# Kernel optimization log

Hardware: AMD Instinct MI355X
Metric: run time of the kernel (lower is better)

The kernel has to match this reference:

```python
import jax, jax.numpy as jnp
import numpy as np

NU, NM, E, H = 200000, 40000, 2000000, 64


def setup_inputs() -> dict:
    key = jax.random.key(0)
    ks = jax.random.split(key, 16)
    inp = {}
    inp["x_user"] = jnp.arange(NU, dtype=jnp.int32)
    inp["x_movie"] = jnp.arange(NM, dtype=jnp.int32)
    # user->movie ratings and the reverse edge type (same edges, flipped)
    src_u = jax.random.randint(ks[0], (E,), 0, NU, dtype=jnp.int32)
    dst_m = jax.random.randint(ks[1], (E,), 0, NM, dtype=jnp.int32)
    inp["edge_src_um"], inp["edge_dst_um"] = src_u, dst_m
    inp["edge_src_mu"], inp["edge_dst_mu"] = dst_m, src_u
    inp["user_table"] = jax.random.normal(ks[2], (NU, H), dtype=jnp.float32)
    inp["movie_table"] = jax.random.normal(ks[3], (NM, H), dtype=jnp.float32)
    s = 1.0 / np.sqrt(H)
    wnames = ["Wl1_um", "Wr1_um", "Wl1_mu", "Wr1_mu", "Wl2_um", "Wr2_um", "Wl2_mu", "Wr2_mu"]
    for i, n in enumerate(wnames):
        inp[n] = jax.random.uniform(ks[4 + i], (H, H), minval=-s, maxval=s, dtype=jnp.float32)
    for i, n in enumerate(["b1_um", "b1_mu", "b2_um", "b2_mu"]):
        inp[n] = jax.random.uniform(ks[12 + i], (H,), minval=-s, maxval=s, dtype=jnp.float32)
    return inp


def sage_conv(x_src, x_dst, src, dst, Wl, Wr, b, n_dst):
    """PyG SAGEConv (bipartite, aggr='mean'): lin_l(mean_j x_j) + lin_r(x_i) + b."""
    msg = x_src[src]                                            # [E, H] gather
    agg = jax.ops.segment_sum(msg, dst, num_segments=n_dst)     # [n_dst, H]
    cnt = jax.ops.segment_sum(jnp.ones((src.shape[0], 1), x_src.dtype), dst,
                              num_segments=n_dst)
    agg = agg / jnp.maximum(cnt, 1.0)                           # mean, 0 for isolated nodes
    return agg @ Wl + x_dst @ Wr + b


def reference(x_user, x_movie, edge_src_um, edge_dst_um, edge_src_mu, edge_dst_mu,
              user_table, movie_table,
              Wl1_um, Wr1_um, Wl1_mu, Wr1_mu, Wl2_um, Wr2_um, Wl2_mu, Wr2_mu,
              b1_um, b1_mu, b2_um, b2_mu):
    u0 = user_table[x_user]    # [NU, H]
    m0 = movie_table[x_movie]  # [NM, H]
    # layer 1 (per edge type; each node type has one incoming edge type, aggr='sum' trivial)
    m1 = jax.nn.relu(sage_conv(u0, m0, edge_src_um, edge_dst_um, Wl1_um, Wr1_um, b1_um, NM))
    u1 = jax.nn.relu(sage_conv(m0, u0, edge_src_mu, edge_dst_mu, Wl1_mu, Wr1_mu, b1_mu, NU))
    # layer 2
    m2 = sage_conv(u1, m1, edge_src_um, edge_dst_um, Wl2_um, Wr2_um, b2_um, NM)
    u2 = sage_conv(m1, u1, edge_src_mu, edge_dst_mu, Wl2_mu, Wr2_mu, b2_mu, NU)
    return (u2, m2)
```

## Files before the change

kernel.cpp:

```cpp
#include <hip/hip_runtime.h>

#define HDIM 64
#define CAP_M 96
#define CAP_U 32
#define OVF_MAX 65536
#define NBIN 512
#define NBLK 2048

typedef __attribute__((ext_vector_type(8))) short bf16x8;
typedef __attribute__((ext_vector_type(4))) float f32x4;

__device__ __forceinline__ float bf2f(unsigned short u) {
  unsigned int x = ((unsigned int)u) << 16;
  return __uint_as_float(x);
}
__device__ __forceinline__ unsigned short f2bf(float f) {
  unsigned int x = __float_as_uint(f);
  unsigned int r = (x + 0x7FFFu + ((x >> 16) & 1u)) >> 16;
  return (unsigned short)r;
}

__device__ __forceinline__ int bin_lo(int b, int Nd) {
  return (int)(((long long)b * Nd + NBIN - 1) >> 9);
}

__global__ __launch_bounds__(256) void k_init(int* __restrict__ meta, int nmeta,
                                              const float* __restrict__ ut,
                                              unsigned short* __restrict__ ub, int n8u,
                                              const float* __restrict__ mt,
                                              unsigned short* __restrict__ mb, int n8m) {
  int bid = blockIdx.x;
  if (bid < 512) {
    int i = bid * 256 + threadIdx.x;
    for (int j = i; j < nmeta; j += 512 * 256) meta[j] = 0;
  } else if (bid < 512 + 2048) {
    int i = (bid - 512) * 256 + threadIdx.x;
    for (int j = i; j < n8u; j += 2048 * 256) {
      const float4* p = (const float4*)(ut + (size_t)j * 8);
      float4 a = p[0], b = p[1];
      uint4 o;
      o.x = (unsigned int)f2bf(a.x) | ((unsigned int)f2bf(a.y) << 16);
      o.y = (unsigned int)f2bf(a.z) | ((unsigned int)f2bf(a.w) << 16);
      o.z = (unsigned int)f2bf(b.x) | ((unsigned int)f2bf(b.y) << 16);
      o.w = (unsigned int)f2bf(b.z) | ((unsigned int)f2bf(b.w) << 16);
      *(uint4*)(ub + (size_t)j * 8) = o;
    }
  } else {
    int i = (bid - 512 - 2048) * 256 + threadIdx.x;
    for (int j = i; j < n8m; j += 512 * 256) {
      const float4* p = (const float4*)(mt + (size_t)j * 8);
      float4 a = p[0], b = p[1];
      uint4 o;
      o.x = (unsigned int)f2bf(a.x) | ((unsigned int)f2bf(a.y) << 16);
      o.y = (unsigned int)f2bf(a.z) | ((unsigned int)f2bf(a.w) << 16);
      o.z = (unsigned int)f2bf(b.x) | ((unsigned int)f2bf(b.y) << 16);
      o.w = (unsigned int)f2bf(b.z) | ((unsigned int)f2bf(b.w) << 16);
      *(uint4*)(mb + (size_t)j * 8) = o;
    }
  }
}

__global__ __launch_bounds__(256) void k_hist2(const int* __restrict__ srcU,
                                               const int* __restrict__ dstM,
                                               int E, int NMd, int NUd,
                                               int* __restrict__ ghM,
                                               int* __restrict__ ghU) {
  __shared__ int hM[NBIN];
  __shared__ int hU[NBIN];
  int t = threadIdx.x;
  hM[t] = 0; hM[t + 256] = 0;
  hU[t] = 0; hU[t + 256] = 0;
  __syncthreads();
  int e4 = (E + 3) >> 2;
  int c4 = (e4 + NBLK - 1) / NBLK;
  int clen = c4 << 2;
  int s = blockIdx.x * clen;
  int epos = s + clen; if (epos > E) epos = E;
  for (int i = s + 4 * t; i < epos; i += 1024) {
    int n = epos - i; if (n > 4) n = 4;
    if (n == 4) {
      int4 d4 = *(const int4*)&dstM[i];
      int4 s4 = *(const int4*)&srcU[i];
      atomicAdd(&hM[(int)((long long)d4.x * NBIN / NMd)], 1);
      atomicAdd(&hM[(int)((long long)d4.y * NBIN / NMd)], 1);
      atomicAdd(&hM[(int)((long long)d4.z * NBIN / NMd)], 1);
      atomicAdd(&hM[(int)((long long)d4.w * NBIN / NMd)], 1);
      atomicAdd(&hU[(int)((long long)s4.x * NBIN / NUd)], 1);
      atomicAdd(&hU[(int)((long long)s4.y * NBIN / NUd)], 1);
      atomicAdd(&hU[(int)((long long)s4.z * NBIN / NUd)], 1);
      atomicAdd(&hU[(int)((long long)s4.w * NBIN / NUd)], 1);
    } else {
      for (int j = 0; j < n; ++j) {
        atomicAdd(&hM[(int)((long long)dstM[i + j] * NBIN / NMd)], 1);
        atomicAdd(&hU[(int)((long long)srcU[i + j] * NBIN / NUd)], 1);
      }
    }
  }
  __syncthreads();
  ghM[(size_t)t * NBLK + blockIdx.x] = hM[t];
  ghM[(size_t)(t + 256) * NBLK + blockIdx.x] = hM[t + 256];
  ghU[(size_t)t * NBLK + blockIdx.x] = hU[t];
  ghU[(size_t)(t + 256) * NBLK + blockIdx.x] = hU[t + 256];
}

__global__ void k_block_sum(const int* __restrict__ in, int* __restrict__ part, int n) {
  __shared__ int s[256];
  int b = blockIdx.x, t = threadIdx.x;
  int base = b * 1024;
  int v = 0;
  for (int i = t; i < 1024; i += 256) {
    int idx = base + i;
    if (idx < n) v += in[idx];
  }
  s[t] = v;
  __syncthreads();
  for (int o = 128; o > 0; o >>= 1) {
    if (t < o) s[t] += s[t + o];
    __syncthreads();
  }
  if (t == 0) part[b] = s[0];
}

__global__ void k_scan_part4(int* __restrict__ part, int nb) {
  __shared__ int s[256];
  int t = threadIdx.x;
  int v[4];
  int sum = 0;
#pragma unroll
  for (int i = 0; i < 4; ++i) {
    int idx = t * 4 + i;
    v[i] = (idx < nb) ? part[idx] : 0;
    sum += v[i];
  }
  s[t] = sum;
  __syncthreads();
  for (int o = 1; o < 256; o <<= 1) {
    int u = (t >= o) ? s[t - o] : 0;
    __syncthreads();
    s[t] += u;
    __syncthreads();
  }
  int excl = s[t] - sum;
#pragma unroll
  for (int i = 0; i < 4; ++i) {
    int idx = t * 4 + i;
    if (idx < nb) { int tmp = v[i]; part[idx] = excl; excl += tmp; }
  }
}

__global__ void k_scan_final(const int* __restrict__ in, const int* __restrict__ part,
                             int* __restrict__ out, int n) {
  __shared__ int s[256];
  int b = blockIdx.x, t = threadIdx.x;
  int base = b * 1024 + t * 4;
  int a[4];
#pragma unroll
  for (int i = 0; i < 4; i++) a[i] = (base + i < n) ? in[base + i] : 0;
  int tsum = a[0] + a[1] + a[2] + a[3];
  s[t] = tsum;
  __syncthreads();
  for (int o = 1; o < 256; o <<= 1) {
    int u = (t >= o) ? s[t - o] : 0;
    __syncthreads();
    s[t] += u;
    __syncthreads();
  }
  int excl = s[t] - tsum + part[b];
#pragma unroll
  for (int i = 0; i < 4; i++) {
    if (base + i < n) out[base + i] = excl;
    excl += a[i];
  }
}

__global__ __launch_bounds__(256) void k_scatter2(const int* __restrict__ srcU,
                                                  const int* __restrict__ dstM,
                                                  int E, int NMd, int NUd,
                                                  const int* __restrict__ offsM,
                                                  const int* __restrict__ offsU,
                                                  unsigned int* __restrict__ binnedM,
                                                  unsigned int* __restrict__ binnedU) {
  __shared__ int lcM[NBIN];
  __shared__ int lcU[NBIN];
  int t = threadIdx.x;
  lcM[t] = offsM[(size_t)t * NBLK + blockIdx.x];
  lcM[t + 256] = offsM[(size_t)(t + 256) * NBLK + blockIdx.x];
  lcU[t] = offsU[(size_t)t * NBLK + blockIdx.x];
  lcU[t + 256] = offsU[(size_t)(t + 256) * NBLK + blockIdx.x];
  __syncthreads();
  int e4 = (E + 3) >> 2;
  int c4 = (e4 + NBLK - 1) / NBLK;
  int clen = c4 << 2;
  int s = blockIdx.x * clen;
  int epos = s + clen; if (epos > E) epos = E;
  for (int i = s + 4 * t; i < epos; i += 1024) {
    int n = epos - i; if (n > 4) n = 4;
    if (n == 4) {
      int4 d4 = *(const int4*)&dstM[i];
      int4 s4 = *(const int4*)&srcU[i];
#pragma unroll
      for (int k = 0; k < 4; ++k) {
        int dd = (k == 0) ? d4.x : (k == 1) ? d4.y : (k == 2) ? d4.z : d4.w;
        int ss = (k == 0) ? s4.x : (k == 1) ? s4.y : (k == 2) ? s4.z : s4.w;
        int bm = (int)((long long)dd * NBIN / NMd);
        int pm = atomicAdd(&lcM[bm], 1);
        binnedM[pm] = ((unsigned int)(dd - bin_lo(bm, NMd)) << 18) | (unsigned int)ss;
        int bu = (int)((long long)ss * NBIN / NUd);
        int pu = atomicAdd(&lcU[bu], 1);
        binnedU[pu] = ((unsigned int)(ss - bin_lo(bu, NUd)) << 18) | (unsigned int)dd;
      }
    } else {
      for (int j = 0; j < n; ++j) {
        int dd = dstM[i + j], ss = srcU[i + j];
        int bm = (int)((long long)dd * NBIN / NMd);
        int pm = atomicAdd(&lcM[bm], 1);
        binnedM[pm] = ((unsigned int)(dd - bin_lo(bm, NMd)) << 18) | (unsigned int)ss;
        int bu = (int)((long long)ss * NBIN / NUd);
        int pu = atomicAdd(&lcU[bu], 1);
        binnedU[pu] = ((unsigned int)(ss - bin_lo(bu, NUd)) << 18) | (unsigned int)dd;
      }
    }
  }
}

template <typename IT>
__global__ __launch_bounds__(256) void k_fillbin(const unsigned int* __restrict__ binned,
                                                 const int* __restrict__ offs,
                                                 int E, int Nd, int cap,
                                                 IT* __restrict__ bkt,
                                                 int* __restrict__ cur,
                                                 int* __restrict__ ovf_cnt,
                                                 int* __restrict__ ovf) {
  __shared__ int lcur[400];
  int b = blockIdx.x;
  int t = threadIdx.x;
  int lo = bin_lo(b, Nd);
  int hi = bin_lo(b + 1, Nd);
  if (b == NBIN - 1) hi = Nd;
  int width = hi - lo;
  for (int i = t; i < width; i += 256) lcur[i] = 0;
  __syncthreads();
  int start = offs[(size_t)b * NBLK];
  int end = (b == NBIN - 1) ? E : offs[(size_t)(b + 1) * NBLK];
  for (int i = start + t; i < end; i += 256) {
    unsigned int p = binned[i];
    int li = (int)(p >> 18);
    int val = (int)(p & 0x3FFFFu);
    int pos = atomicAdd(&lcur[li], 1);
    if (pos < cap) bkt[(size_t)(lo + li) * cap + pos] = (IT)val;
    else { int q = atomicAdd(ovf_cnt, 1); if (q < OVF_MAX) { ovf[2 * q] = lo + li; ovf[2 * q + 1] = val; } }
  }
  __syncthreads();
  for (int i = t; i < width; i += 256) cur[lo + i] = lcur[i];
}

__device__ __forceinline__ void acc8(float4& a, float4& b, uint4 w) {
  a.x += __uint_as_float(w.x << 16);
  a.y += __uint_as_float(w.x & 0xFFFF0000u);
  a.z += __uint_as_float(w.y << 16);
  a.w += __uint_as_float(w.y & 0xFFFF0000u);
  b.x += __uint_as_float(w.z << 16);
  b.y += __uint_as_float(w.z & 0xFFFF0000u);
  b.z += __uint_as_float(w.w << 16);
  b.w += __uint_as_float(w.w & 0xFFFF0000u);
}

template <typename IT>
__global__ __launch_bounds__(256) void k_agg8(const unsigned short* __restrict__ xb,
                                              const int* __restrict__ cur,
                                              const IT* __restrict__ bkt,
                                              int cap,
                                              float* __restrict__ agg,
                                              int n_dst) {
  int t = threadIdx.x;
  int q = t & 7;
  int gg = (blockIdx.x * 256 + t) >> 3;
  int stride = (gridDim.x * 256) >> 3;

  for (int node = gg; node < n_dst; node += stride) {
    int deg = cur[node];
    int nb = deg < cap ? deg : cap;
    const IT* lst = bkt + (size_t)node * cap;
    float4 a = make_float4(0.f, 0.f, 0.f, 0.f);
    float4 b = a;
    int e = 0;
    for (; e + 4 <= nb; e += 4) {
      int i0, i1, i2, i3;
      if (sizeof(IT) == 2) {
        ushort4 ia = *(const ushort4*)&lst[e];
        i0 = ia.x; i1 = ia.y; i2 = ia.z; i3 = ia.w;
      } else {
        int4 ia = *(const int4*)&lst[e];
        i0 = ia.x; i1 = ia.y; i2 = ia.z; i3 = ia.w;
      }
      uint4 w0 = *(const uint4*)&xb[(size_t)i0 * HDIM + 8 * q];
      uint4 w1 = *(const uint4*)&xb[(size_t)i1 * HDIM + 8 * q];
      uint4 w2 = *(const uint4*)&xb[(size_t)i2 * HDIM + 8 * q];
      uint4 w3 = *(const uint4*)&xb[(size_t)i3 * HDIM + 8 * q];
      acc8(a, b, w0);
      acc8(a, b, w1);
      acc8(a, b, w2);
      acc8(a, b, w3);
    }
    for (; e < nb; ++e) {
      uint4 w0 = *(const uint4*)&xb[(size_t)lst[e] * HDIM + 8 * q];
      acc8(a, b, w0);
    }
    float inv = deg > 0 ? 1.f / (float)deg : 0.f;
    a.x *= inv; a.y *= inv; a.z *= inv; a.w *= inv;
    b.x *= inv; b.y *= inv; b.z *= inv; b.w *= inv;
    *(float4*)&agg[(size_t)node * HDIM + 8 * q] = a;
    *(float4*)&agg[(size_t)node * HDIM + 8 * q + 4] = b;
  }
}

__device__ __forceinline__ void fix_body(const int* __restrict__ cnt_p,
                                         const int* __restrict__ ovf,
                                         const unsigned short* __restrict__ xb,
                                         const int* __restrict__ cur,
                                         float* __restrict__ agg,
                                         int bid, int nblk) {
  int n = *cnt_p;
  if (n > OVF_MAX) n = OVF_MAX;
  int tid = bid * 256 + threadIdx.x;
  int q = tid & 15;
  int p = tid >> 4;
  int stride = (nblk * 256) >> 4;
  for (; p < n; p += stride) {
    int d = ovf[2 * p];
    int s = ovf[2 * p + 1];
    float inv = 1.f / (float)cur[d];
    ushort4 v = *(const ushort4*)&xb[(size_t)s * HDIM + 4 * q];
    atomicAdd(&agg[(size_t)d * HDIM + 4 * q + 0], bf2f(v.x) * inv);
    atomicAdd(&agg[(size_t)d * HDIM + 4 * q + 1], bf2f(v.y) * inv);
    atomicAdd(&agg[(size_t)d * HDIM + 4 * q + 2], bf2f(v.z) * inv);
    atomicAdd(&agg[(size_t)d * HDIM + 4 * q + 3], bf2f(v.w) * inv);
  }
}

__global__ __launch_bounds__(256) void k_fix2(const int* __restrict__ cntM,
                                              const int* __restrict__ ovfM,
                                              const unsigned short* __restrict__ xbM,
                                              const int* __restrict__ curM,
                                              float* __restrict__ aggM,
                                              const int* __restrict__ cntU,
                                              const int* __restrict__ ovfU,
                                              const unsigned short* __restrict__ xbU,
                                              const int* __restrict__ curU,
                                              float* __restrict__ aggU) {
  if (blockIdx.x < 16) fix_body(cntM, ovfM, xbM, curM, aggM, blockIdx.x, 16);
  else                 fix_body(cntU, ovfU, xbU, curU, aggU, blockIdx.x - 16, 16);
}

template <int OUTBF>
__global__ __launch_bounds__(256) void k_xmfma(const float* A,
                                               const unsigned short* X,
                                               const float* __restrict__ Wl,
                                               const float* __restrict__ Wr,
                                               const float* __restrict__ bias,
                                               void* outv,
                                               int n_dst, int do_relu) {
  __shared__ unsigned short sWt[64][136];
  __shared__ float sOut[4][16][68];

  int t = threadIdx.x;
  for (int id = t; id < 64 * 128; id += 256) {
    int col = id & 63;
    int k = id >> 6;
    float wv = (k < 64) ? Wl[k * 64 + col] : Wr[(k - 64) * 64 + col];
    sWt[col][k] = f2bf(wv);
  }
  __syncthreads();

  int w = t >> 6;
  int l = t & 63;
  int lm = l & 15;
  int lg = l >> 4;
  int wid = blockIdx.x * 4 + w;
  int nw = gridDim.x * 4;
  int ntiles = (n_dst + 15) >> 4;

  for (int tile = wid; tile < ntiles; tile += nw) {
    int nbase = tile << 4;
    int row = nbase + lm;
    int rowc = row < n_dst ? row : (n_dst - 1);

    bf16x8 afr[4];
    const float* ar = A + (size_t)rowc * HDIM;
#pragma unroll
    for (int s = 0; s < 2; ++s) {
      float4 f0 = *(const float4*)(ar + 32 * s + 8 * lg);
      float4 f1 = *(const float4*)(ar + 32 * s + 8 * lg + 4);
      bf16x8 v;
      v[0] = (short)f2bf(f0.x); v[1] = (short)f2bf(f0.y);
      v[2] = (short)f2bf(f0.z); v[3] = (short)f2bf(f0.w);
      v[4] = (short)f2bf(f1.x); v[5] = (short)f2bf(f1.y);
      v[6] = (short)f2bf(f1.z); v[7] = (short)f2bf(f1.w);
      afr[s] = v;
    }
    const unsigned short* xr = X + (size_t)rowc * HDIM;
#pragma unroll
    for (int s = 0; s < 2; ++s) {
      afr[2 + s] = *(const bf16x8*)(xr + 32 * s + 8 * lg);
    }

    f32x4 zz = {0.f, 0.f, 0.f, 0.f};
    f32x4 acc[4];
#pragma unroll
    for (int n = 0; n < 4; ++n) acc[n] = zz;
#pragma unroll
    for (int s = 0; s < 4; ++s) {
#pragma unroll
      for (int n = 0; n < 4; ++n) {
        bf16x8 bfr = *(const bf16x8*)(&sWt[16 * n + lm][32 * s + 8 * lg]);
        acc[n] = __builtin_amdgcn_mfma_f32_16x16x32_bf16(afr[s], bfr, acc[n], 0, 0, 0);
      }
    }

#pragma unroll
    for (int n = 0; n < 4; ++n) {
      float bj = bias[16 * n + lm];
#pragma unroll
      for (int r = 0; r < 4; ++r) {
        float v = acc[n][r] + bj;
        if (do_relu) v = fmaxf(v, 0.f);
        sOut[w][lg * 4 + r][16 * n + lm] = v;
      }
    }

    int node = nbase + (l >> 2);
    if (node < n_dst) {
      int c0 = (l & 3) * 16;
      float4 o0 = *(const float4*)&sOut[w][l >> 2][c0];
      float4 o1 = *(const float4*)&sOut[w][l >> 2][c0 + 4];
      float4 o2 = *(const float4*)&sOut[w][l >> 2][c0 + 8];
      float4 o3 = *(const float4*)&sOut[w][l >> 2][c0 + 12];
      if (OUTBF) {
        unsigned short* ob = (unsigned short*)outv;
        uint4 p0, p1;
        p0.x = (unsigned int)f2bf(o0.x) | ((unsigned int)f2bf(o0.y) << 16);
        p0.y = (unsigned int)f2bf(o0.z) | ((unsigned int)f2bf(o0.w) << 16);
        p0.z = (unsigned int)f2bf(o1.x) | ((unsigned int)f2bf(o1.y) << 16);
        p0.w = (unsigned int)f2bf(o1.z) | ((unsigned int)f2bf(o1.w) << 16);
        p1.x = (unsigned int)f2bf(o2.x) | ((unsigned int)f2bf(o2.y) << 16);
        p1.y = (unsigned int)f2bf(o2.z) | ((unsigned int)f2bf(o2.w) << 16);
        p1.z = (unsigned int)f2bf(o3.x) | ((unsigned int)f2bf(o3.y) << 16);
        p1.w = (unsigned int)f2bf(o3.z) | ((unsigned int)f2bf(o3.w) << 16);
        *(uint4*)&ob[(size_t)node * HDIM + c0] = p0;
        *(uint4*)&ob[(size_t)node * HDIM + c0 + 8] = p1;
      } else {
        float* of = (float*)outv;
        *(float4*)&of[(size_t)node * HDIM + c0] = o0;
        *(float4*)&of[(size_t)node * HDIM + c0 + 4] = o1;
        *(float4*)&of[(size_t)node * HDIM + c0 + 8] = o2;
        *(float4*)&of[(size_t)node * HDIM + c0 + 12] = o3;
      }
    }
  }
}


static inline int imin(int a, int b) { return a < b ? a : b; }

extern "C" void kernel_launch(void* const* d_in, const int* in_sizes, int n_in,
                              void* d_out, int out_size, void* d_ws, size_t ws_size,
                              hipStream_t stream) {
  const int NU = in_sizes[0];
  const int NM = in_sizes[1];
  const int E  = in_sizes[2];

  const int* src_um = (const int*)d_in[2];
  const int* dst_um = (const int*)d_in[3];
  const float* user_table  = (const float*)d_in[6];
  const float* movie_table = (const float*)d_in[7];
  const float* Wl1_um = (const float*)d_in[8];
  const float* Wr1_um = (const float*)d_in[9];
  const float* Wl1_mu = (const float*)d_in[10];
  const float* Wr1_mu = (const float*)d_in[11];
  const float* Wl2_um = (const float*)d_in[12];
  const float* Wr2_um = (const float*)d_in[13];
  const float* Wl2_mu = (const float*)d_in[14];
  const float* Wr2_mu = (const float*)d_in[15];
  const float* b1_um = (const float*)d_in[16];
  const float* b1_mu = (const float*)d_in[17];
  const float* b2_um = (const float*)d_in[18];
  const float* b2_mu = (const float*)d_in[19];

  float* out_u2 = (float*)d_out;
  float* out_m2 = (float*)d_out + (size_t)NU * HDIM;
  float* aggu = out_u2;
  float* aggm = out_m2;
  unsigned int* binnedM = (unsigned int*)d_out;
  unsigned int* binnedU = (unsigned int*)d_out + E;

  char* ws = (char*)d_ws;
  size_t off = 0;
  auto carve = [&](size_t bytes) -> char* {
    char* p = ws + off;
    off = (off + bytes + 255) & ~(size_t)255;
    return p;
  };
  int* meta = (int*)carve((size_t)(NM + NU + 2) * 4);
  int* curm = meta;
  int* curu = meta + NM;
  int* ovfm_cnt = meta + NM + NU;
  int* ovfu_cnt = meta + NM + NU + 1;
  int nmeta = NM + NU + 2;
  int* ovfm = (int*)carve((size_t)OVF_MAX * 2 * 4);
  int* ovfu = (int*)carve((size_t)OVF_MAX * 2 * 4);
  int* bktm = (int*)carve((size_t)NM * CAP_M * 4);
  unsigned short* bktu = (unsigned short*)carve((size_t)NU * CAP_U * 2);
  unsigned short* mb = (unsigned short*)carve((size_t)NM * HDIM * 2);
  unsigned short* ub = (unsigned short*)carve((size_t)NU * HDIM * 2);
  int* ghM = (int*)carve((size_t)NBIN * NBLK * 4);
  int* ghU = (int*)carve((size_t)NBIN * NBLK * 4);
  int* part = (int*)carve(1024 * 4);
  (void)ws_size;

  const int TB = 256;
  int nscan = NBIN * NBLK;
  int nbscan = (nscan + 1023) / 1024;

  int n8u = NU * HDIM / 8, n8m = NM * HDIM / 8;
  k_init<<<3072, TB, 0, stream>>>(meta, nmeta, user_table, ub, n8u,
                                  movie_table, mb, n8m);

  k_hist2<<<NBLK, TB, 0, stream>>>(src_um, dst_um, E, NM, NU, ghM, ghU);
  k_block_sum<<<nbscan, TB, 0, stream>>>(ghM, part, nscan);
  k_scan_part4<<<1, TB, 0, stream>>>(part, nbscan);
  k_scan_final<<<nbscan, TB, 0, stream>>>(ghM, part, ghM, nscan);
  k_block_sum<<<nbscan, TB, 0, stream>>>(ghU, part, nscan);
  k_scan_part4<<<1, TB, 0, stream>>>(part, nbscan);
  k_scan_final<<<nbscan, TB, 0, stream>>>(ghU, part, ghU, nscan);
  k_scatter2<<<NBLK, TB, 0, stream>>>(src_um, dst_um, E, NM, NU,
                                      ghM, ghU, binnedM, binnedU);
  k_fillbin<int><<<NBIN, TB, 0, stream>>>(binnedM, ghM, E, NM, CAP_M,
                                          bktm, curm, ovfm_cnt, ovfm);
  k_fillbin<unsigned short><<<NBIN, TB, 0, stream>>>(binnedU, ghU, E, NU, CAP_U,
                                                     bktu, curu, ovfu_cnt, ovfu);

  int gAm = imin((NM + 31) / 32, 8192);
  int gAu = imin((NU + 31) / 32, 8192);
  int gXm = (NM + 63) / 64;
  int gXu = (NU + 63) / 64;

  k_agg8<int><<<gAm, TB, 0, stream>>>(ub, curm, bktm, CAP_M, aggm, NM);
  k_agg8<unsigned short><<<gAu, TB, 0, stream>>>(mb, curu, bktu, CAP_U, aggu, NU);
  k_fix2<<<32, TB, 0, stream>>>(ovfm_cnt, ovfm, ub, curm, aggm,
                                ovfu_cnt, ovfu, mb, curu, aggu);
  k_xmfma<1><<<gXm, TB, 0, stream>>>(aggm, mb, Wl1_um, Wr1_um, b1_um,
                                     mb, NM, 1);
  k_xmfma<1><<<gXu, TB, 0, stream>>>(aggu, ub, Wl1_mu, Wr1_mu, b1_mu,
                                     ub, NU, 1);

  k_agg8<int><<<gAm, TB, 0, stream>>>(ub, curm, bktm, CAP_M, aggm, NM);
  k_agg8<unsigned short><<<gAu, TB, 0, stream>>>(mb, curu, bktu, CAP_U, aggu, NU);
  k_fix2<<<32, TB, 0, stream>>>(ovfm_cnt, ovfm, ub, curm, aggm,
                                ovfu_cnt, ovfu, mb, curu, aggu);
  k_xmfma<0><<<gXm, TB, 0, stream>>>(aggm, mb, Wl2_um, Wr2_um, b2_um,
                                     out_m2, NM, 0);
  k_xmfma<0><<<gXu, TB, 0, stream>>>(aggu, ub, Wl2_mu, Wr2_mu, b2_mu,
                                     out_u2, NU, 0);
}
```

Before: 377.2 us.

## Reduce histogram blocks and pad per-block bin segments to 16-entry alignment

Cuts the histogram/scatter grid from 2048 to 512 blocks, which shrinks the per-bin-per-block offset table and lets the top-level scan run in a single pass. Each block's bin segment is padded up to a multiple of 16 entries and the tail is filled with sentinel values, so scatter writes land in aligned chunks; fillbin skips the sentinels. The binned buffers grow, and the U buffer is placed at a fixed offset of 6.3M words inside the output buffer. Scan results now go to separate arrays so the raw counts stay available to compute the end of the last bin.

```diff
diff --git a/kernel.cpp b/kernel.cpp
--- a/kernel.cpp
+++ b/kernel.cpp
@@ -5,7 +5,8 @@
 #define CAP_U 32
 #define OVF_MAX 65536
 #define NBIN 512
-#define NBLK 2048
+#define NBLK 512
+#define SENT 0xFFFFFFFFu
 
 typedef __attribute__((ext_vector_type(8))) short bf16x8;
 typedef __attribute__((ext_vector_type(4))) float f32x4;
@@ -19,6 +20,7 @@
   unsigned int r = (x + 0x7FFFu + ((x >> 16) & 1u)) >> 16;
   return (unsigned short)r;
 }
+__device__ __forceinline__ int rup16(int x) { return (x + 15) & ~15; }
 
 __device__ __forceinline__ int bin_lo(int b, int Nd) {
   return (int)(((long long)b * Nd + NBIN - 1) >> 9);
@@ -103,6 +105,7 @@
   ghU[(size_t)(t + 256) * NBLK + blockIdx.x] = hU[t + 256];
 }
 
+template <int PAD>
 __global__ void k_block_sum(const int* __restrict__ in, int* __restrict__ part, int n) {
   __shared__ int s[256];
   int b = blockIdx.x, t = threadIdx.x;
@@ -110,7 +113,7 @@
   int v = 0;
   for (int i = t; i < 1024; i += 256) {
     int idx = base + i;
-    if (idx < n) v += in[idx];
+    if (idx < n) v += PAD ? rup16(in[idx]) : in[idx];
   }
   s[t] = v;
   __syncthreads();
@@ -121,18 +124,11 @@
   if (t == 0) part[b] = s[0];
 }
 
-__global__ void k_scan_part4(int* __restrict__ part, int nb) {
+__global__ void k_scan_part(int* __restrict__ part, int nb) {
   __shared__ int s[256];
   int t = threadIdx.x;
-  int v[4];
-  int sum = 0;
-#pragma unroll
-  for (int i = 0; i < 4; ++i) {
-    int idx = t * 4 + i;
-    v[i] = (idx < nb) ? part[idx] : 0;
-    sum += v[i];
-  }
-  s[t] = sum;
+  int v = (t < nb) ? part[t] : 0;
+  s[t] = v;
   __syncthreads();
   for (int o = 1; o < 256; o <<= 1) {
     int u = (t >= o) ? s[t - o] : 0;
@@ -140,14 +136,10 @@
     s[t] += u;
     __syncthreads();
   }
-  int excl = s[t] - sum;
-#pragma unroll
-  for (int i = 0; i < 4; ++i) {
-    int idx = t * 4 + i;
-    if (idx < nb) { int tmp = v[i]; part[idx] = excl; excl += tmp; }
-  }
-}
-
+  if (t < nb) part[t] = s[t] - v;
+}
+
+template <int PAD>
 __global__ void k_scan_final(const int* __restrict__ in, const int* __restrict__ part,
                              int* __restrict__ out, int n) {
   __shared__ int s[256];
@@ -155,7 +147,10 @@
   int base = b * 1024 + t * 4;
   int a[4];
 #pragma unroll
-  for (int i = 0; i < 4; i++) a[i] = (base + i < n) ? in[base + i] : 0;
+  for (int i = 0; i < 4; i++) {
+    int idx = base + i;
+    a[i] = (idx < n) ? (PAD ? rup16(in[idx]) : in[idx]) : 0;
+  }
   int tsum = a[0] + a[1] + a[2] + a[3];
   s[t] = tsum;
   __syncthreads();
@@ -221,11 +216,25 @@
       }
     }
   }
+  __syncthreads();
+#pragma unroll
+  for (int rep = 0; rep < 2; ++rep) {
+    int bin = t + rep * 256;
+    int s0 = offsM[(size_t)bin * NBLK + blockIdx.x];
+    int fin = lcM[bin];
+    int pe = s0 + rup16(fin - s0);
+    for (int i = fin; i < pe; ++i) binnedM[i] = SENT;
+    s0 = offsU[(size_t)bin * NBLK + blockIdx.x];
+    fin = lcU[bin];
+    pe = s0 + rup16(fin - s0);
+    for (int i = fin; i < pe; ++i) binnedU[i] = SENT;
+  }
 }
 
 template <typename IT>
 __global__ __launch_bounds__(256) void k_fillbin(const unsigned int* __restrict__ binned,
                                                  const int* __restrict__ offs,
+                                                 const int* __restrict__ ghraw,
                                                  int E, int Nd, int cap,
                                                  IT* __restrict__ bkt,
                                                  int* __restrict__ cur,
@@ -241,9 +250,17 @@
   for (int i = t; i < width; i += 256) lcur[i] = 0;
   __syncthreads();
   int start = offs[(size_t)b * NBLK];
-  int end = (b == NBIN - 1) ? E : offs[(size_t)(b + 1) * NBLK];
+  int end;
+  if (b == NBIN - 1) {
+    int lastoff = offs[(size_t)NBIN * NBLK - 1];
+    int lastcnt = ghraw[(size_t)NBIN * NBLK - 1];
+    end = lastoff + rup16(lastcnt);
+  } else {
+    end = offs[(size_t)(b + 1) * NBLK];
+  }
   for (int i = start + t; i < end; i += 256) {
     unsigned int p = binned[i];
+    if (p == SENT) continue;
     int li = (int)(p >> 18);
     int val = (int)(p & 0x3FFFFu);
     int pos = atomicAdd(&lcur[li], 1);
@@ -491,7 +508,7 @@
   float* aggu = out_u2;
   float* aggm = out_m2;
   unsigned int* binnedM = (unsigned int*)d_out;
-  unsigned int* binnedU = (unsigned int*)d_out + E;
+  unsigned int* binnedU = (unsigned int*)d_out + 6300000;
 
   char* ws = (char*)d_ws;
   size_t off = 0;
@@ -512,9 +529,11 @@
   unsigned short* bktu = (unsigned short*)carve((size_t)NU * CAP_U * 2);
   unsigned short* mb = (unsigned short*)carve((size_t)NM * HDIM * 2);
   unsigned short* ub = (unsigned short*)carve((size_t)NU * HDIM * 2);
-  int* ghM = (int*)carve((size_t)NBIN * NBLK * 4);
-  int* ghU = (int*)carve((size_t)NBIN * NBLK * 4);
-  int* part = (int*)carve(1024 * 4);
+  int* ghM  = (int*)carve((size_t)NBIN * NBLK * 4);
+  int* ghsM = (int*)carve((size_t)NBIN * NBLK * 4);
+  int* ghU  = (int*)carve((size_t)NBIN * NBLK * 4);
+  int* ghsU = (int*)carve((size_t)NBIN * NBLK * 4);
+  int* part = (int*)carve(256 * 4);
   (void)ws_size;
 
   const int TB = 256;
@@ -526,17 +545,17 @@
                                   movie_table, mb, n8m);
 
   k_hist2<<<NBLK, TB, 0, stream>>>(src_um, dst_um, E, NM, NU, ghM, ghU);
-  k_block_sum<<<nbscan, TB, 0, stream>>>(ghM, part, nscan);
-  k_scan_part4<<<1, TB, 0, stream>>>(part, nbscan);
-  k_scan_final<<<nbscan, TB, 0, stream>>>(ghM, part, ghM, nscan);
-  k_block_sum<<<nbscan, TB, 0, stream>>>(ghU, part, nscan);
-  k_scan_part4<<<1, TB, 0, stream>>>(part, nbscan);
-  k_scan_final<<<nbscan, TB, 0, stream>>>(ghU, part, ghU, nscan);
+  k_block_sum<1><<<nbscan, TB, 0, stream>>>(ghM, part, nscan);
+  k_scan_part<<<1, TB, 0, stream>>>(part, nbscan);
+  k_scan_final<1><<<nbscan, TB, 0, stream>>>(ghM, part, ghsM, nscan);
+  k_block_sum<1><<<nbscan, TB, 0, stream>>>(ghU, part, nscan);
+  k_scan_part<<<1, TB, 0, stream>>>(part, nbscan);
+  k_scan_final<1><<<nbscan, TB, 0, stream>>>(ghU, part, ghsU, nscan);
   k_scatter2<<<NBLK, TB, 0, stream>>>(src_um, dst_um, E, NM, NU,
-                                      ghM, ghU, binnedM, binnedU);
-  k_fillbin<int><<<NBIN, TB, 0, stream>>>(binnedM, ghM, E, NM, CAP_M,
+                                      ghsM, ghsU, binnedM, binnedU);
+  k_fillbin<int><<<NBIN, TB, 0, stream>>>(binnedM, ghsM, ghM, E, NM, CAP_M,
                                           bktm, curm, ovfm_cnt, ovfm);
-  k_fillbin<unsigned short><<<NBIN, TB, 0, stream>>>(binnedU, ghU, E, NU, CAP_U,
+  k_fillbin<unsigned short><<<NBIN, TB, 0, stream>>>(binnedU, ghsU, ghU, E, NU, CAP_U,
                                                      bktu, curu, ovfu_cnt, ovfu);
 
   int gAm = imin((NM + 31) / 32, 8192);
```

Result: no change. 373.3 us (-1.0%).

## Merge M/U scan and fillbin launches, shrink histogram blocks, store binned pairs unpacked

Applied to the files above, without the earlier changes.

Cuts the histogram block count from 2048 to 512, which shrinks the per-block offset tables. The two separate three-kernel scans for the movie and user histograms become one combined three-kernel scan that writes into separate output buffers, and the two fillbin launches become one. Binned edges are stored as int2 (dst, src) pairs instead of packed 32-bit words, which removes the bin-relative packing but doubles the binned traffic. Fewer blocks also means less parallelism in the hist and scatter passes.

```diff
diff --git a/kernel.cpp b/kernel.cpp
--- a/kernel.cpp
+++ b/kernel.cpp
@@ -5,7 +5,7 @@
 #define CAP_U 32
 #define OVF_MAX 65536
 #define NBIN 512
-#define NBLK 2048
+#define NBLK 512
 
 typedef __attribute__((ext_vector_type(8))) short bf16x8;
 typedef __attribute__((ext_vector_type(4))) float f32x4;
@@ -18,10 +18,6 @@
   unsigned int x = __float_as_uint(f);
   unsigned int r = (x + 0x7FFFu + ((x >> 16) & 1u)) >> 16;
   return (unsigned short)r;
-}
-
-__device__ __forceinline__ int bin_lo(int b, int Nd) {
-  return (int)(((long long)b * Nd + NBIN - 1) >> 9);
 }
 
 __global__ __launch_bounds__(256) void k_init(int* __restrict__ meta, int nmeta,
@@ -103,10 +99,13 @@
   ghU[(size_t)(t + 256) * NBLK + blockIdx.x] = hU[t + 256];
 }
 
-__global__ void k_block_sum(const int* __restrict__ in, int* __restrict__ part, int n) {
+__global__ void k_block_sum2(const int* __restrict__ ghM, const int* __restrict__ ghU,
+                             int* __restrict__ part, int n) {
   __shared__ int s[256];
   int b = blockIdx.x, t = threadIdx.x;
-  int base = b * 1024;
+  const int* in = (b < 256) ? ghM : ghU;
+  int cb = (b < 256) ? b : (b - 256);
+  int base = cb * 1024;
   int v = 0;
   for (int i = t; i < 1024; i += 256) {
     int idx = base + i;
@@ -121,18 +120,39 @@
   if (t == 0) part[b] = s[0];
 }
 
-__global__ void k_scan_part4(int* __restrict__ part, int nb) {
+__global__ void k_scan_part2(int* __restrict__ part) {
   __shared__ int s[256];
   int t = threadIdx.x;
-  int v[4];
-  int sum = 0;
-#pragma unroll
-  for (int i = 0; i < 4; ++i) {
-    int idx = t * 4 + i;
-    v[i] = (idx < nb) ? part[idx] : 0;
-    sum += v[i];
-  }
-  s[t] = sum;
+#pragma unroll
+  for (int half = 0; half < 2; ++half) {
+    int v = part[half * 256 + t];
+    s[t] = v;
+    __syncthreads();
+    for (int o = 1; o < 256; o <<= 1) {
+      int u = (t >= o) ? s[t - o] : 0;
+      __syncthreads();
+      s[t] += u;
+      __syncthreads();
+    }
+    part[half * 256 + t] = s[t] - v;
+    __syncthreads();
+  }
+}
+
+__global__ void k_scan_final2(const int* __restrict__ ghM, const int* __restrict__ ghU,
+                              const int* __restrict__ part,
+                              int* __restrict__ ghsM, int* __restrict__ ghsU, int n) {
+  __shared__ int s[256];
+  int b = blockIdx.x, t = threadIdx.x;
+  const int* in = (b < 256) ? ghM : ghU;
+  int* out = (b < 256) ? ghsM : ghsU;
+  int cb = (b < 256) ? b : (b - 256);
+  int base = cb * 1024 + t * 4;
+  int a[4];
+#pragma unroll
+  for (int i = 0; i < 4; i++) a[i] = (base + i < n) ? in[base + i] : 0;
+  int tsum = a[0] + a[1] + a[2] + a[3];
+  s[t] = tsum;
   __syncthreads();
   for (int o = 1; o < 256; o <<= 1) {
     int u = (t >= o) ? s[t - o] : 0;
@@ -140,31 +160,6 @@
     s[t] += u;
     __syncthreads();
   }
-  int excl = s[t] - sum;
-#pragma unroll
-  for (int i = 0; i < 4; ++i) {
-    int idx = t * 4 + i;
-    if (idx < nb) { int tmp = v[i]; part[idx] = excl; excl += tmp; }
-  }
-}
-
-__global__ void k_scan_final(const int* __restrict__ in, const int* __restrict__ part,
-                             int* __restrict__ out, int n) {
-  __shared__ int s[256];
-  int b = blockIdx.x, t = threadIdx.x;
-  int base = b * 1024 + t * 4;
-  int a[4];
-#pragma unroll
-  for (int i = 0; i < 4; i++) a[i] = (base + i < n) ? in[base + i] : 0;
-  int tsum = a[0] + a[1] + a[2] + a[3];
-  s[t] = tsum;
-  __syncthreads();
-  for (int o = 1; o < 256; o <<= 1) {
-    int u = (t >= o) ? s[t - o] : 0;
-    __syncthreads();
-    s[t] += u;
-    __syncthreads();
-  }
   int excl = s[t] - tsum + part[b];
 #pragma unroll
   for (int i = 0; i < 4; i++) {
@@ -178,8 +173,8 @@
                                                   int E, int NMd, int NUd,
                                                   const int* __restrict__ offsM,
                                                   const int* __restrict__ offsU,
-                                                  unsigned int* __restrict__ binnedM,
-                                                  unsigned int* __restrict__ binnedU) {
+                                                  int2* __restrict__ binnedM,
+                                                  int2* __restrict__ binnedU) {
   __shared__ int lcM[NBIN];
   __shared__ int lcU[NBIN];
   int t = threadIdx.x;
@@ -204,38 +199,37 @@
         int ss = (k == 0) ? s4.x : (k == 1) ? s4.y : (k == 2) ? s4.z : s4.w;
         int bm = (int)((long long)dd * NBIN / NMd);
         int pm = atomicAdd(&lcM[bm], 1);
-        binnedM[pm] = ((unsigned int)(dd - bin_lo(bm, NMd)) << 18) | (unsigned int)ss;
+        binnedM[pm] = make_int2(dd, ss);
         int bu = (int)((long long)ss * NBIN / NUd);
         int pu = atomicAdd(&lcU[bu], 1);
-        binnedU[pu] = ((unsigned int)(ss - bin_lo(bu, NUd)) << 18) | (unsigned int)dd;
+        binnedU[pu] = make_int2(ss, dd);
       }
     } else {
       for (int j = 0; j < n; ++j) {
         int dd = dstM[i + j], ss = srcU[i + j];
         int bm = (int)((long long)dd * NBIN / NMd);
         int pm = atomicAdd(&lcM[bm], 1);
-        binnedM[pm] = ((unsigned int)(dd - bin_lo(bm, NMd)) << 18) | (unsigned int)ss;
+        binnedM[pm] = make_int2(dd, ss);
         int bu = (int)((long long)ss * NBIN / NUd);
         int pu = atomicAdd(&lcU[bu], 1);
-        binnedU[pu] = ((unsigned int)(ss - bin_lo(bu, NUd)) << 18) | (unsigned int)dd;
+        binnedU[pu] = make_int2(ss, dd);
       }
     }
   }
 }
 
 template <typename IT>
-__global__ __launch_bounds__(256) void k_fillbin(const unsigned int* __restrict__ binned,
-                                                 const int* __restrict__ offs,
-                                                 int E, int Nd, int cap,
-                                                 IT* __restrict__ bkt,
-                                                 int* __restrict__ cur,
-                                                 int* __restrict__ ovf_cnt,
-                                                 int* __restrict__ ovf) {
-  __shared__ int lcur[400];
-  int b = blockIdx.x;
+__device__ __forceinline__ void fillbin_body(const int2* __restrict__ binned,
+                                             const int* __restrict__ offs,
+                                             int b, int E, int Nd, int cap,
+                                             IT* __restrict__ bkt,
+                                             int* __restrict__ cur,
+                                             int* __restrict__ ovf_cnt,
+                                             int* __restrict__ ovf,
+                                             int* lcur) {
   int t = threadIdx.x;
-  int lo = bin_lo(b, Nd);
-  int hi = bin_lo(b + 1, Nd);
+  int lo = (int)(((long long)b * Nd + NBIN - 1) >> 9);
+  int hi = (int)(((long long)(b + 1) * Nd + NBIN - 1) >> 9);
   if (b == NBIN - 1) hi = Nd;
   int width = hi - lo;
   for (int i = t; i < width; i += 256) lcur[i] = 0;
@@ -243,15 +237,36 @@
   int start = offs[(size_t)b * NBLK];
   int end = (b == NBIN - 1) ? E : offs[(size_t)(b + 1) * NBLK];
   for (int i = start + t; i < end; i += 256) {
-    unsigned int p = binned[i];
-    int li = (int)(p >> 18);
-    int val = (int)(p & 0x3FFFFu);
+    int2 p = binned[i];
+    int li = p.x - lo;
     int pos = atomicAdd(&lcur[li], 1);
-    if (pos < cap) bkt[(size_t)(lo + li) * cap + pos] = (IT)val;
-    else { int q = atomicAdd(ovf_cnt, 1); if (q < OVF_MAX) { ovf[2 * q] = lo + li; ovf[2 * q + 1] = val; } }
+    if (pos < cap) bkt[(size_t)p.x * cap + pos] = (IT)p.y;
+    else { int q = atomicAdd(ovf_cnt, 1); if (q < OVF_MAX) { ovf[2 * q] = p.x; ovf[2 * q + 1] = p.y; } }
   }
   __syncthreads();
   for (int i = t; i < width; i += 256) cur[lo + i] = lcur[i];
+}
+
+__global__ __launch_bounds__(256) void k_fillbin2(const int2* __restrict__ binnedM,
+                                                  const int* __restrict__ offsM,
+                                                  int NMd, int* __restrict__ bktM,
+                                                  int* __restrict__ curM,
+                                                  int* __restrict__ ovfM_cnt,
+                                                  int* __restrict__ ovfM,
+                                                  const int2* __restrict__ binnedU,
+                                                  const int* __restrict__ offsU,
+                                                  int NUd, unsigned short* __restrict__ bktU,
+                                                  int* __restrict__ curU,
+                                                  int* __restrict__ ovfU_cnt,
+                                                  int* __restrict__ ovfU,
+                                                  int E) {
+  __shared__ int lcur[400];
+  int b = blockIdx.x;
+  if (b < NBIN)
+    fillbin_body<int>(binnedM, offsM, b, E, NMd, CAP_M, bktM, curM, ovfM_cnt, ovfM, lcur);
+  else
+    fillbin_body<unsigned short>(binnedU, offsU, b - NBIN, E, NUd, CAP_U,
+                                 bktU, curU, ovfU_cnt, ovfU, lcur);
 }
 
 __device__ __forceinline__ void acc8(float4& a, float4& b, uint4 w) {
@@ -490,8 +505,8 @@
   float* out_m2 = (float*)d_out + (size_t)NU * HDIM;
   float* aggu = out_u2;
   float* aggm = out_m2;
-  unsigned int* binnedM = (unsigned int*)d_out;
-  unsigned int* binnedU = (unsigned int*)d_out + E;
+  int2* binnedM = (int2*)d_out;
+  int2* binnedU = (int2*)d_out + E;
 
   char* ws = (char*)d_ws;
   size_t off = 0;
@@ -512,32 +527,28 @@
   unsigned short* bktu = (unsigned short*)carve((size_t)NU * CAP_U * 2);
   unsigned short* mb = (unsigned short*)carve((size_t)NM * HDIM * 2);
   unsigned short* ub = (unsigned short*)carve((size_t)NU * HDIM * 2);
-  int* ghM = (int*)carve((size_t)NBIN * NBLK * 4);
-  int* ghU = (int*)carve((size_t)NBIN * NBLK * 4);
-  int* part = (int*)carve(1024 * 4);
+  int* ghM  = (int*)carve((size_t)NBIN * NBLK * 4);
+  int* ghsM = (int*)carve((size_t)NBIN * NBLK * 4);
+  int* ghU  = (int*)carve((size_t)NBIN * NBLK * 4);
+  int* ghsU = (int*)carve((size_t)NBIN * NBLK * 4);
+  int* part = (int*)carve(512 * 4);
   (void)ws_size;
 
   const int TB = 256;
   int nscan = NBIN * NBLK;
-  int nbscan = (nscan + 1023) / 1024;
 
   int n8u = NU * HDIM / 8, n8m = NM * HDIM / 8;
   k_init<<<3072, TB, 0, stream>>>(meta, nmeta, user_table, ub, n8u,
                                   movie_table, mb, n8m);
 
   k_hist2<<<NBLK, TB, 0, stream>>>(src_um, dst_um, E, NM, NU, ghM, ghU);
-  k_block_sum<<<nbscan, TB, 0, stream>>>(ghM, part, nscan);
-  k_scan_part4<<<1, TB, 0, stream>>>(part, nbscan);
-  k_scan_final<<<nbscan, TB, 0, stream>>>(ghM, part, ghM, nscan);
-  k_block_sum<<<nbscan, TB, 0, stream>>>(ghU, part, nscan);
-  k_scan_part4<<<1, TB, 0, stream>>>(part, nbscan);
-  k_scan_final<<<nbscan, TB, 0, stream>>>(ghU, part, ghU, nscan);
+  k_block_sum2<<<512, TB, 0, stream>>>(ghM, ghU, part, nscan);
+  k_scan_part2<<<1, TB, 0, stream>>>(part);
+  k_scan_final2<<<512, TB, 0, stream>>>(ghM, ghU, part, ghsM, ghsU, nscan);
   k_scatter2<<<NBLK, TB, 0, stream>>>(src_um, dst_um, E, NM, NU,
-                                      ghM, ghU, binnedM, binnedU);
-  k_fillbin<int><<<NBIN, TB, 0, stream>>>(binnedM, ghM, E, NM, CAP_M,
-                                          bktm, curm, ovfm_cnt, ovfm);
-  k_fillbin<unsigned short><<<NBIN, TB, 0, stream>>>(binnedU, ghU, E, NU, CAP_U,
-                                                     bktu, curu, ovfu_cnt, ovfu);
+                                      ghsM, ghsU, binnedM, binnedU);
+  k_fillbin2<<<2 * NBIN, TB, 0, stream>>>(binnedM, ghsM, NM, bktm, curm, ovfm_cnt, ovfm,
+                                          binnedU, ghsU, NU, bktu, curu, ovfu_cnt, ovfu, E);
 
   int gAm = imin((NM + 31) / 32, 8192);
   int gAu = imin((NU + 31) / 32, 8192);
```

New measurement: 344.1 us. 8.8% less time.
